# Performance work log

Measured on AMD Instinct MI355X. Metric: run time of the kernel, lower is better.

## Reference

```python
import jax, jax.numpy as jnp
import numpy as np

B, N = 8, 16384
NPOINT, RADIUS, NSAMPLE, IN_CH = 512, 0.5, 64, 6
EPS = 1e-5


def _sqdist(a, b):
    # a [B,S,3], b [B,N,3] -> [B,S,N] squared euclidean distances
    return (jnp.sum(a * a, -1)[:, :, None] + jnp.sum(b * b, -1)[:, None, :]
            - 2.0 * jnp.einsum('bsd,bnd->bsn', a, b))


def _fps(xyz, npoint):
    # farthest point sampling (deterministic: starts from index 0)
    Bb, Nn, _ = xyz.shape
    def body(carry, _):
        dist, far = carry  # dist [B,N], far [B]
        centroid = jnp.take_along_axis(xyz, far[:, None, None], axis=1)  # [B,1,3]
        d = jnp.sum((xyz - centroid) ** 2, -1)
        dist = jnp.minimum(dist, d)
        return (dist, jnp.argmax(dist, -1).astype(jnp.int32)), far
    init = (jnp.full((Bb, Nn), 1e10, xyz.dtype), jnp.zeros((Bb,), jnp.int32))
    _, idx = jax.lax.scan(body, init, None, length=npoint)
    return idx.T  # [B, npoint]


def _ball_query(radius, nsample, xyz, new_xyz):
    Nn = xyz.shape[1]
    sq = _sqdist(new_xyz, xyz)  # [B,S,N]
    gidx = jnp.where(sq > radius * radius, Nn,
                     jnp.arange(Nn, dtype=jnp.int32)[None, None, :])
    gidx = jnp.sort(gidx, axis=-1)[:, :, :nsample]  # [B,S,K]
    # pad slots (==N) get the first valid index, as in reference torch code
    return jnp.where(gidx == Nn, gidx[:, :, :1], gidx)


def _gather(x, idx):
    # x [B,N,C], idx [B,...] -> [B,...,C]
    return jax.vmap(lambda xb, ib: xb[ib])(x, idx)


def _forward(xyz, points, layers):
    fps_idx = _fps(xyz, NPOINT)
    new_xyz = _gather(xyz, fps_idx)                        # [B,S,3]
    idx = _ball_query(RADIUS, NSAMPLE, xyz, new_xyz)       # [B,S,K]
    grouped_xyz = _gather(xyz, idx) - new_xyz[:, :, None]  # [B,S,K,3]
    grouped_pts = _gather(points, idx)                     # [B,S,K,3]
    h = jnp.concatenate([grouped_xyz, grouped_pts], -1)[..., :IN_CH]  # [B,S,K,6]
    for (W, b, g, beta) in layers:
        # 1x1 Conv2d == per-point linear; BatchNorm2d (train mode) over (B,K,S)
        h = jnp.einsum('bskc,oc->bsko', h, W) + b
        mu = jnp.mean(h, axis=(0, 1, 2))
        var = jnp.var(h, axis=(0, 1, 2))
        h = jax.nn.relu(g * (h - mu) * jax.lax.rsqrt(var + EPS) + beta)
    return new_xyz, jnp.max(h, axis=2)  # [B,S,3], [B,S,C_out]


def setup_inputs() -> dict:
    key = jax.random.key(0)
    ks = jax.random.split(key, 4)
    return {
        'xyz': jax.random.normal(ks[0], (B, N, 3), jnp.float32),
        'points': jax.random.normal(ks[1], (B, N, 3), jnp.float32),
        'W0': jax.random.normal(ks[2], (64, IN_CH), jnp.float32) * (1.0 / np.sqrt(IN_CH)),
        'b0': jnp.zeros((64,), jnp.float32),
        'g0': jnp.ones((64,), jnp.float32),
        'beta0': jnp.zeros((64,), jnp.float32),
        'W1': jax.random.normal(ks[3], (128, 64), jnp.float32) * (1.0 / np.sqrt(64)),
        'b1': jnp.zeros((128,), jnp.float32),
        'g1': jnp.ones((128,), jnp.float32),
        'beta1': jnp.zeros((128,), jnp.float32),
    }


def reference(xyz, points, W0, b0, g0, beta0, W1, b1, g1, beta1):
    layers = [(W0, b0, g0, beta0), (W1, b1, g1, beta1)]
    return _forward(xyz, points, layers)
```

## Files before the change

### kernel.cpp

```cpp
#include <hip/hip_runtime.h>

#define NB    8
#define NPTS  16384
#define NS    512
#define NK    64
#define C1    64
#define C2    128
#define RAD2  0.25f
#define MTOT  (NB*NS*NK)

typedef float v2f __attribute__((ext_vector_type(2)));
typedef __bf16 bfv8 __attribute__((ext_vector_type(8)));
typedef float f32x4 __attribute__((ext_vector_type(4)));

extern __shared__ char dynsmem[];

#define UMAX_DPP(x, CTRL, RM)                                                   \
    do {                                                                        \
        unsigned _m = (unsigned)__builtin_amdgcn_update_dpp((int)(x), (int)(x), \
                                                            CTRL, RM, 0xf, false); \
        x = (x > _m) ? x : _m;                                                  \
    } while (0)
#define UMIN_DPP(x, CTRL, RM)                                                   \
    do {                                                                        \
        unsigned _m = (unsigned)__builtin_amdgcn_update_dpp((int)(x), (int)(x), \
                                                            CTRL, RM, 0xf, false); \
        x = (x < _m) ? x : _m;                                                  \
    } while (0)

__global__ __launch_bounds__(1024, 4) void fps_kernel(const float* __restrict__ xyz,
                                                      float* __restrict__ out) {
#pragma clang fp contract(off)
    int b = blockIdx.x;
    int tid = threadIdx.x;
    int lane = tid & 63;
    int w = tid >> 6;
    const float* base = xyz + (size_t)b * NPTS * 3;
    v2f* yv = (v2f*)dynsmem;
    v2f* zv = yv + 8192;
    __shared__ unsigned svals[2][16];
    __shared__ unsigned sidxs[2][16];
    v2f pxp[8], ddp[8];
#pragma unroll
    for (int jj = 0; jj < 8; ++jj) {
        int p0 = tid + (jj << 11);
        int p1 = p0 + 1024;
        float x0 = base[p0 * 3 + 0], y0 = base[p0 * 3 + 1], z0 = base[p0 * 3 + 2];
        float x1 = base[p1 * 3 + 0], y1 = base[p1 * 3 + 1], z1 = base[p1 * 3 + 2];
        pxp[jj].x = x0; pxp[jj].y = x1;
        v2f yp; yp.x = y0; yp.y = y1;
        v2f zp; zp.x = z0; zp.y = z1;
        yv[(jj << 10) + tid] = yp;
        zv[(jj << 10) + tid] = zp;
        ddp[jj].x = 1e10f; ddp[jj].y = 1e10f;
    }
    float cx = base[0], cy = base[1], cz = base[2];
    if (tid == 0) {
        float* o = out + (size_t)b * NS * 3;
        o[0] = cx; o[1] = cy; o[2] = cz;
    }
    __syncthreads();
    for (int i = 1; i < NS; ++i) {
        v2f cx2; cx2.x = cx; cx2.y = cx;
        v2f cy2; cy2.x = cy; cy2.y = cy;
        v2f cz2; cz2.x = cz; cz2.y = cz;
        v2f cm0, cm1, cm2, cm3;
        cm0.x = -1.f; cm0.y = -1.f; cm1 = cm0; cm2 = cm0; cm3 = cm0;
#pragma unroll
        for (int jj = 0; jj < 8; ++jj) {
            v2f yp = yv[(jj << 10) + tid];
            v2f zp = zv[(jj << 10) + tid];
            v2f dx = pxp[jj] - cx2;
            v2f dy = yp - cy2;
            v2f dz = zp - cz2;
            v2f d = (dx * dx + dy * dy) + dz * dz;
            v2f nd;
            nd.x = fminf(ddp[jj].x, d.x);
            nd.y = fminf(ddp[jj].y, d.y);
            ddp[jj] = nd;
            if ((jj & 3) == 0) { cm0.x = fmaxf(cm0.x, nd.x); cm0.y = fmaxf(cm0.y, nd.y); }
            if ((jj & 3) == 1) { cm1.x = fmaxf(cm1.x, nd.x); cm1.y = fmaxf(cm1.y, nd.y); }
            if ((jj & 3) == 2) { cm2.x = fmaxf(cm2.x, nd.x); cm2.y = fmaxf(cm2.y, nd.y); }
            if ((jj & 3) == 3) { cm3.x = fmaxf(cm3.x, nd.x); cm3.y = fmaxf(cm3.y, nd.y); }
        }
        v2f m01; m01.x = fmaxf(cm0.x, cm1.x); m01.y = fmaxf(cm0.y, cm1.y);
        v2f m23; m23.x = fmaxf(cm2.x, cm3.x); m23.y = fmaxf(cm2.y, cm3.y);
        float bv = fmaxf(fmaxf(m01.x, m23.x), fmaxf(m01.y, m23.y));
        unsigned vb = (unsigned)__float_as_int(bv);
        UMAX_DPP(vb, 0xB1, 0xf);
        UMAX_DPP(vb, 0x4E, 0xf);
        UMAX_DPP(vb, 0x141, 0xf);
        UMAX_DPP(vb, 0x140, 0xf);
        UMAX_DPP(vb, 0x142, 0xa);
        UMAX_DPP(vb, 0x143, 0xc);
        if (lane == 63) svals[i & 1][w] = vb;
        __syncthreads();
        unsigned wv = svals[i & 1][lane & 15];
        UMAX_DPP(wv, 0xB1, 0xf);
        UMAX_DPP(wv, 0x4E, 0xf);
        UMAX_DPP(wv, 0x141, 0xf);
        UMAX_DPP(wv, 0x140, 0xf);
        float W = __int_as_float((int)wv);
        unsigned lidx = 0x7fffffffu;
        if (__any(bv == W)) {
#pragma unroll
            for (int jj = 7; jj >= 0; --jj) {
                if (ddp[jj].y == W) lidx = (unsigned)(tid + (jj << 11) + 1024);
                if (ddp[jj].x == W) lidx = (unsigned)(tid + (jj << 11));
            }
        }
        UMIN_DPP(lidx, 0xB1, 0xf);
        UMIN_DPP(lidx, 0x4E, 0xf);
        UMIN_DPP(lidx, 0x141, 0xf);
        UMIN_DPP(lidx, 0x140, 0xf);
        UMIN_DPP(lidx, 0x142, 0xa);
        UMIN_DPP(lidx, 0x143, 0xc);
        if (lane == 63) sidxs[i & 1][w] = lidx;
        __syncthreads();
        unsigned ci = sidxs[i & 1][lane & 15];
        UMIN_DPP(ci, 0xB1, 0xf);
        UMIN_DPP(ci, 0x4E, 0xf);
        UMIN_DPP(ci, 0x141, 0xf);
        UMIN_DPP(ci, 0x140, 0xf);
        int ii = __builtin_amdgcn_readfirstlane((int)ci);
        const float* cp = base + (size_t)ii * 3;
        cx = cp[0]; cy = cp[1]; cz = cp[2];
        if (tid == 0) {
            float* o = out + ((size_t)b * NS + i) * 3;
            o[0] = cx; o[1] = cy; o[2] = cz;
        }
    }
}

__global__ __launch_bounds__(256) void ballq_kernel(const float* __restrict__ xyz,
                                                    const float* __restrict__ pts,
                                                    const float* __restrict__ newxyz,
                                                    float* __restrict__ feat) {
    int w = threadIdx.x >> 6;
    int lane = threadIdx.x & 63;
    int wid = blockIdx.x * 4 + w;
    int b = wid >> 9;
    const float* nx = newxyz + (size_t)wid * 3;
    float cx = nx[0], cy = nx[1], cz = nx[2];
    float sa = __fadd_rn(__fadd_rn(__fmul_rn(cx, cx), __fmul_rn(cy, cy)),
                         __fmul_rn(cz, cz));
    __shared__ int sidx[4][64];
    const float* base = xyz + (size_t)b * NPTS * 3;
    int cnt = 0;
    for (int off = 0; off < NPTS && cnt < NK; off += 64) {
        int p = off + lane;
        float bx = base[p * 3 + 0], by = base[p * 3 + 1], bz = base[p * 3 + 2];
        float sb = __fadd_rn(__fadd_rn(__fmul_rn(bx, bx), __fmul_rn(by, by)),
                             __fmul_rn(bz, bz));
        float dt = __fadd_rn(__fadd_rn(__fmul_rn(cx, bx), __fmul_rn(cy, by)),
                             __fmul_rn(cz, bz));
        float sq = __fsub_rn(__fadd_rn(sa, sb), __fmul_rn(2.0f, dt));
        bool inb = !(sq > RAD2);
        unsigned long long mask = __ballot(inb);
        int pos = cnt + (int)__popcll(mask & ((1ull << lane) - 1ull));
        if (inb && pos < NK) sidx[w][pos] = p;
        cnt += (int)__popcll(mask);
    }
    __syncthreads();
    int filled = cnt < NK ? cnt : NK;
    int sel = (lane < filled) ? lane : 0;
    int p = (filled > 0) ? sidx[w][sel] : 0;
    float gx = base[p * 3 + 0], gy = base[p * 3 + 1], gz = base[p * 3 + 2];
    const float* pb = pts + (size_t)b * NPTS * 3;
    float q0 = pb[p * 3 + 0], q1 = pb[p * 3 + 1], q2 = pb[p * 3 + 2];
    float* fr = feat + ((size_t)wid * NK + lane) * 6;
    fr[0] = __fsub_rn(gx, cx);
    fr[1] = __fsub_rn(gy, cy);
    fr[2] = __fsub_rn(gz, cz);
    fr[3] = q0; fr[4] = q1; fr[5] = q2;
}

__global__ __launch_bounds__(256) void stats0_kernel(const float* __restrict__ feat,
                                                     const float* __restrict__ W0,
                                                     const float* __restrict__ b0,
                                                     float* __restrict__ stats) {
    int lane = threadIdx.x & 63;
    int wid = blockIdx.x * 4 + (threadIdx.x >> 6);
    float w0[6];
#pragma unroll
    for (int j = 0; j < 6; ++j) w0[j] = W0[lane * 6 + j];
    float bb = b0[lane];
    float ssum = 0.f, ssq = 0.f;
    int r0 = wid * 256;
    for (int r = r0; r < r0 + 256; ++r) {
        const float* f = feat + (size_t)r * 6;
        float h = bb;
#pragma unroll
        for (int j = 0; j < 6; ++j) h = fmaf(w0[j], f[j], h);
        ssum += h;
        ssq = fmaf(h, h, ssq);
    }
    atomicAdd(&stats[lane], ssum);
    atomicAdd(&stats[64 + lane], ssq);
}

__device__ __forceinline__ void bf16_split(float v, unsigned short& hi, unsigned short& lo) {
    unsigned u = __float_as_uint(v);
    unsigned h = (u + 0x7fffu + ((u >> 16) & 1u)) >> 16;
    float rem = v - __uint_as_float(h << 16);
    unsigned ur = __float_as_uint(rem);
    unsigned l = (ur + 0x7fffu + ((ur >> 16) & 1u)) >> 16;
    hi = (unsigned short)h; lo = (unsigned short)l;
}

__global__ __launch_bounds__(256) void stats1_mfma_kernel(const float* __restrict__ feat,
                                                          const float* __restrict__ W0,
                                                          const float* __restrict__ b0,
                                                          const float* __restrict__ W1,
                                                          const float* __restrict__ b1,
                                                          const float* __restrict__ g0,
                                                          const float* __restrict__ be0,
                                                          float* __restrict__ stats) {
    char* lds = dynsmem;
    int tid = threadIdx.x;
    int lane = tid & 63;
    int w = tid >> 6;
    int g = blockIdx.x * 4 + w;
    for (int idx = tid; idx < 8192; idx += 256) {
        int o = idx >> 6, c = idx & 63;
        unsigned short hi, lo;
        bf16_split(W1[idx], hi, lo);
        int byt = (c * 2) ^ ((o & 7) << 4);
        *(unsigned short*)(lds + o * 128 + byt) = hi;
        *(unsigned short*)(lds + 16384 + o * 128 + byt) = lo;
    }
    const float inv = 1.0f / (float)MTOT;
    float mu0 = stats[lane] * inv;
    float var0 = fmaxf(stats[64 + lane] * inv - mu0 * mu0, 0.f);
    float a0 = g0[lane] * rsqrtf(var0 + 1e-5f);
    float c0v = fmaf(-mu0, a0, be0[lane]);
    float w0r[6];
#pragma unroll
    for (int j = 0; j < 6; ++j) w0r[j] = W0[lane * 6 + j];
    float b0v = b0[lane];
    char* X = lds + 32768 + w * 16384;
    __syncthreads();
    const float* fb = feat + (size_t)g * 64 * 6;
#pragma unroll 4
    for (int r = 0; r < 64; ++r) {
        const float* f = fb + r * 6;
        float h = b0v;
#pragma unroll
        for (int j = 0; j < 6; ++j) h = fmaf(w0r[j], f[j], h);
        float hn = fmaxf(fmaf(a0, h, c0v), 0.f);
        unsigned short hi, lo;
        bf16_split(hn, hi, lo);
        int byt = (lane * 2) ^ ((r & 7) << 4);
        *(unsigned short*)(X + r * 128 + byt) = hi;
        *(unsigned short*)(X + 8192 + r * 128 + byt) = lo;
    }
    __syncthreads();
    float b1v[8];
#pragma unroll
    for (int tn = 0; tn < 8; ++tn) b1v[tn] = b1[tn * 16 + (lane & 15)];
    float ssum[8], ssq[8];
#pragma unroll
    for (int tn = 0; tn < 8; ++tn) { ssum[tn] = 0.f; ssq[tn] = 0.f; }
#pragma unroll
    for (int tm = 0; tm < 4; ++tm) {
        bfv8 Ah[2], Al[2];
#pragma unroll
        for (int tk = 0; tk < 2; ++tk) {
            int r = tm * 16 + (lane & 15);
            int colb = (((lane >> 4) * 16) + tk * 64) ^ ((r & 7) << 4);
            Ah[tk] = *(const bfv8*)(X + r * 128 + colb);
            Al[tk] = *(const bfv8*)(X + 8192 + r * 128 + colb);
        }
#pragma unroll
        for (int tn = 0; tn < 8; ++tn) {
            int o = tn * 16 + (lane & 15);
            f32x4 acc = {0.f, 0.f, 0.f, 0.f};
#pragma unroll
            for (int tk = 0; tk < 2; ++tk) {
                int colb = (((lane >> 4) * 16) + tk * 64) ^ ((o & 7) << 4);
                bfv8 Bh = *(const bfv8*)(lds + o * 128 + colb);
                bfv8 Bl = *(const bfv8*)(lds + 16384 + o * 128 + colb);
                acc = __builtin_amdgcn_mfma_f32_16x16x32_bf16(Ah[tk], Bh, acc, 0, 0, 0);
                acc = __builtin_amdgcn_mfma_f32_16x16x32_bf16(Ah[tk], Bl, acc, 0, 0, 0);
                acc = __builtin_amdgcn_mfma_f32_16x16x32_bf16(Al[tk], Bh, acc, 0, 0, 0);
            }
#pragma unroll
            for (int j = 0; j < 4; ++j) {
                float h1 = acc[j] + b1v[tn];
                ssum[tn] += h1;
                ssq[tn] = fmaf(h1, h1, ssq[tn]);
            }
        }
    }
#pragma unroll
    for (int tn = 0; tn < 8; ++tn) {
        ssum[tn] += __shfl_xor(ssum[tn], 16);
        ssum[tn] += __shfl_xor(ssum[tn], 32);
        ssq[tn] += __shfl_xor(ssq[tn], 16);
        ssq[tn] += __shfl_xor(ssq[tn], 32);
    }
    __syncthreads();
    float* psum = (float*)(lds + 32768);
    float* psq  = (float*)(lds + 32768 + 4096);
    if (lane < 16) {
#pragma unroll
        for (int tn = 0; tn < 8; ++tn) {
            psum[w * 256 + tn * 16 + lane] = ssum[tn];
            psq[w * 256 + tn * 16 + lane] = ssq[tn];
        }
    }
    __syncthreads();
    {
        int ch = tid;
        if (ch < 128) {
            float s = psum[ch] + psum[256 + ch] + psum[512 + ch] + psum[768 + ch];
            float q = psq[ch] + psq[256 + ch] + psq[512 + ch] + psq[768 + ch];
            atomicAdd(&stats[128 + ch], s);
            atomicAdd(&stats[256 + ch], q);
        }
    }
}

__global__ __launch_bounds__(256) void final_mfma_kernel(const float* __restrict__ feat,
                                                         const float* __restrict__ W0,
                                                         const float* __restrict__ b0,
                                                         const float* __restrict__ W1,
                                                         const float* __restrict__ b1,
                                                         const float* __restrict__ g0,
                                                         const float* __restrict__ be0,
                                                         const float* __restrict__ g1,
                                                         const float* __restrict__ be1,
                                                         const float* __restrict__ stats,
                                                         float* __restrict__ out) {
    char* lds = dynsmem;
    int tid = threadIdx.x;
    int lane = tid & 63;
    int w = tid >> 6;
    int g = blockIdx.x * 4 + w;
    for (int idx = tid; idx < 8192; idx += 256) {
        int o = idx >> 6, c = idx & 63;
        unsigned short hi, lo;
        bf16_split(W1[idx], hi, lo);
        int byt = (c * 2) ^ ((o & 7) << 4);
        *(unsigned short*)(lds + o * 128 + byt) = hi;
        *(unsigned short*)(lds + 16384 + o * 128 + byt) = lo;
    }
    const float inv = 1.0f / (float)MTOT;
    float mu0 = stats[lane] * inv;
    float var0 = fmaxf(stats[64 + lane] * inv - mu0 * mu0, 0.f);
    float a0 = g0[lane] * rsqrtf(var0 + 1e-5f);
    float c0v = fmaf(-mu0, a0, be0[lane]);
    float w0r[6];
#pragma unroll
    for (int j = 0; j < 6; ++j) w0r[j] = W0[lane * 6 + j];
    float b0v = b0[lane];
    char* X = lds + 32768 + w * 16384;
    __syncthreads();
    const float* fb = feat + (size_t)g * 64 * 6;
#pragma unroll 4
    for (int r = 0; r < 64; ++r) {
        const float* f = fb + r * 6;
        float h = b0v;
#pragma unroll
        for (int j = 0; j < 6; ++j) h = fmaf(w0r[j], f[j], h);
        float hn = fmaxf(fmaf(a0, h, c0v), 0.f);
        unsigned short hi, lo;
        bf16_split(hn, hi, lo);
        int byt = (lane * 2) ^ ((r & 7) << 4);
        *(unsigned short*)(X + r * 128 + byt) = hi;
        *(unsigned short*)(X + 8192 + r * 128 + byt) = lo;
    }
    __syncthreads();
    float a1v[8], d1v[8];
#pragma unroll
    for (int tn = 0; tn < 8; ++tn) {
        int o = tn * 16 + (lane & 15);
        float mu1 = stats[128 + o] * inv;
        float var1 = fmaxf(stats[256 + o] * inv - mu1 * mu1, 0.f);
        float a1 = g1[o] * rsqrtf(var1 + 1e-5f);
        float c1 = fmaf(-mu1, a1, be1[o]);
        a1v[tn] = a1;
        d1v[tn] = fmaf(a1, b1[o], c1);
    }
    float mx[8];
#pragma unroll
    for (int tn = 0; tn < 8; ++tn) mx[tn] = -1e30f;
#pragma unroll
    for (int tm = 0; tm < 4; ++tm) {
        bfv8 Ah[2], Al[2];
#pragma unroll
        for (int tk = 0; tk < 2; ++tk) {
            int r = tm * 16 + (lane & 15);
            int colb = (((lane >> 4) * 16) + tk * 64) ^ ((r & 7) << 4);
            Ah[tk] = *(const bfv8*)(X + r * 128 + colb);
            Al[tk] = *(const bfv8*)(X + 8192 + r * 128 + colb);
        }
#pragma unroll
        for (int tn = 0; tn < 8; ++tn) {
            int o = tn * 16 + (lane & 15);
            f32x4 acc = {0.f, 0.f, 0.f, 0.f};
#pragma unroll
            for (int tk = 0; tk < 2; ++tk) {
                int colb = (((lane >> 4) * 16) + tk * 64) ^ ((o & 7) << 4);
                bfv8 Bh = *(const bfv8*)(lds + o * 128 + colb);
                bfv8 Bl = *(const bfv8*)(lds + 16384 + o * 128 + colb);
                acc = __builtin_amdgcn_mfma_f32_16x16x32_bf16(Ah[tk], Bh, acc, 0, 0, 0);
                acc = __builtin_amdgcn_mfma_f32_16x16x32_bf16(Ah[tk], Bl, acc, 0, 0, 0);
                acc = __builtin_amdgcn_mfma_f32_16x16x32_bf16(Al[tk], Bh, acc, 0, 0, 0);
            }
            float t0 = fmaxf(fmaf(a1v[tn], acc[0], d1v[tn]), 0.f);
            float t1 = fmaxf(fmaf(a1v[tn], acc[1], d1v[tn]), 0.f);
            float t2 = fmaxf(fmaf(a1v[tn], acc[2], d1v[tn]), 0.f);
            float t3 = fmaxf(fmaf(a1v[tn], acc[3], d1v[tn]), 0.f);
            mx[tn] = fmaxf(mx[tn], fmaxf(fmaxf(t0, t1), fmaxf(t2, t3)));
        }
    }
#pragma unroll
    for (int tn = 0; tn < 8; ++tn) {
        float v = mx[tn];
        v = fmaxf(v, __shfl_xor(v, 16));
        v = fmaxf(v, __shfl_xor(v, 32));
        mx[tn] = v;
    }
    if (lane < 16) {
        size_t ob = 12288 + (size_t)g * 128;
#pragma unroll
        for (int tn = 0; tn < 8; ++tn) out[ob + tn * 16 + lane] = mx[tn];
    }
}

extern "C" void kernel_launch(void* const* d_in, const int* in_sizes, int n_in,
                              void* d_out, int out_size, void* d_ws, size_t ws_size,
                              hipStream_t stream) {
    const float* xyz = (const float*)d_in[0];
    const float* pts = (const float*)d_in[1];
    const float* W0  = (const float*)d_in[2];
    const float* b0  = (const float*)d_in[3];
    const float* g0  = (const float*)d_in[4];
    const float* be0 = (const float*)d_in[5];
    const float* W1  = (const float*)d_in[6];
    const float* b1  = (const float*)d_in[7];
    const float* g1  = (const float*)d_in[8];
    const float* be1 = (const float*)d_in[9];
    float* out = (float*)d_out;

    float* feat  = (float*)d_ws;
    float* stats = feat + (size_t)MTOT * 6;

    const int fps_lds = 2 * NPTS * (int)sizeof(float);
    (void)hipFuncSetAttribute(reinterpret_cast<const void*>(fps_kernel),
                              hipFuncAttributeMaxDynamicSharedMemorySize, fps_lds);
    const int fm_lds = 98304;
    (void)hipFuncSetAttribute(reinterpret_cast<const void*>(stats1_mfma_kernel),
                              hipFuncAttributeMaxDynamicSharedMemorySize, fm_lds);
    (void)hipFuncSetAttribute(reinterpret_cast<const void*>(final_mfma_kernel),
                              hipFuncAttributeMaxDynamicSharedMemorySize, fm_lds);

    (void)hipMemsetAsync(stats, 0, 384 * sizeof(float), stream);
    fps_kernel<<<NB, 1024, fps_lds, stream>>>(xyz, out);
    ballq_kernel<<<1024, 256, 0, stream>>>(xyz, pts, out, feat);
    stats0_kernel<<<256, 256, 0, stream>>>(feat, W0, b0, stats);
    stats1_mfma_kernel<<<1024, 256, fm_lds, stream>>>(feat, W0, b0, W1, b1, g0, be0, stats);
    final_mfma_kernel<<<1024, 256, fm_lds, stream>>>(feat, W0, b0, W1, b1, g0, be0, g1, be1, stats, out);
}
```

Baseline: 1.064 ms.

## Derive layer-0 BatchNorm stats from input moments fused into ball query

Removes the separate stats0 kernel, which reread the whole feature buffer to compute per-channel sum and sum of squares of the first linear layer. The ball-query kernel now accumulates first and second moments of the 6-channel input (27 values) with DPP wave reductions and one atomic per block. The downstream kernels reconstruct layer-0 mean and variance algebraically from W0, b0 and these moments. This saves a kernel launch and a full pass over feat, at the cost of extra reductions in ball query and different floating-point accumulation, which may shift the variance slightly.

```diff
diff --git a/kernel.cpp b/kernel.cpp
--- a/kernel.cpp
+++ b/kernel.cpp
@@ -26,6 +26,12 @@
         unsigned _m = (unsigned)__builtin_amdgcn_update_dpp((int)(x), (int)(x), \
                                                             CTRL, RM, 0xf, false); \
         x = (x < _m) ? x : _m;                                                  \
+    } while (0)
+#define FSUM_DPP(x, CTRL, RM)                                                   \
+    do {                                                                        \
+        int _b = __builtin_amdgcn_update_dpp(0, __float_as_int(x), CTRL, RM,    \
+                                             0xf, false);                       \
+        x += __int_as_float(_b);                                                \
     } while (0)
 
 __global__ __launch_bounds__(1024, 4) void fps_kernel(const float* __restrict__ xyz,
@@ -135,7 +141,8 @@
 __global__ __launch_bounds__(256) void ballq_kernel(const float* __restrict__ xyz,
                                                     const float* __restrict__ pts,
                                                     const float* __restrict__ newxyz,
-                                                    float* __restrict__ feat) {
+                                                    float* __restrict__ feat,
+                                                    float* __restrict__ stats) {
     int w = threadIdx.x >> 6;
     int lane = threadIdx.x & 63;
     int wid = blockIdx.x * 4 + w;
@@ -145,6 +152,7 @@
     float sa = __fadd_rn(__fadd_rn(__fmul_rn(cx, cx), __fmul_rn(cy, cy)),
                          __fmul_rn(cz, cz));
     __shared__ int sidx[4][64];
+    __shared__ float pm[4][27];
     const float* base = xyz + (size_t)b * NPTS * 3;
     int cnt = 0;
     for (int off = 0; off < NPTS && cnt < NK; off += 64) {
@@ -167,36 +175,42 @@
     int p = (filled > 0) ? sidx[w][sel] : 0;
     float gx = base[p * 3 + 0], gy = base[p * 3 + 1], gz = base[p * 3 + 2];
     const float* pb = pts + (size_t)b * NPTS * 3;
-    float q0 = pb[p * 3 + 0], q1 = pb[p * 3 + 1], q2 = pb[p * 3 + 2];
+    float rowf[6];
+    rowf[0] = __fsub_rn(gx, cx);
+    rowf[1] = __fsub_rn(gy, cy);
+    rowf[2] = __fsub_rn(gz, cz);
+    rowf[3] = pb[p * 3 + 0];
+    rowf[4] = pb[p * 3 + 1];
+    rowf[5] = pb[p * 3 + 2];
     float* fr = feat + ((size_t)wid * NK + lane) * 6;
-    fr[0] = __fsub_rn(gx, cx);
-    fr[1] = __fsub_rn(gy, cy);
-    fr[2] = __fsub_rn(gz, cz);
-    fr[3] = q0; fr[4] = q1; fr[5] = q2;
-}
-
-__global__ __launch_bounds__(256) void stats0_kernel(const float* __restrict__ feat,
-                                                     const float* __restrict__ W0,
-                                                     const float* __restrict__ b0,
-                                                     float* __restrict__ stats) {
-    int lane = threadIdx.x & 63;
-    int wid = blockIdx.x * 4 + (threadIdx.x >> 6);
-    float w0[6];
-#pragma unroll
-    for (int j = 0; j < 6; ++j) w0[j] = W0[lane * 6 + j];
-    float bb = b0[lane];
-    float ssum = 0.f, ssq = 0.f;
-    int r0 = wid * 256;
-    for (int r = r0; r < r0 + 256; ++r) {
-        const float* f = feat + (size_t)r * 6;
-        float h = bb;
-#pragma unroll
-        for (int j = 0; j < 6; ++j) h = fmaf(w0[j], f[j], h);
-        ssum += h;
-        ssq = fmaf(h, h, ssq);
-    }
-    atomicAdd(&stats[lane], ssum);
-    atomicAdd(&stats[64 + lane], ssq);
+#pragma unroll
+    for (int j = 0; j < 6; ++j) fr[j] = rowf[j];
+    float mom[27];
+#pragma unroll
+    for (int j = 0; j < 6; ++j) mom[j] = rowf[j];
+    {
+        int t = 6;
+#pragma unroll
+        for (int j = 0; j < 6; ++j)
+#pragma unroll
+            for (int k = j; k < 6; ++k) mom[t++] = rowf[j] * rowf[k];
+    }
+#pragma unroll
+    for (int t = 0; t < 27; ++t) {
+        FSUM_DPP(mom[t], 0xB1, 0xf);
+        FSUM_DPP(mom[t], 0x4E, 0xf);
+        FSUM_DPP(mom[t], 0x141, 0xf);
+        FSUM_DPP(mom[t], 0x140, 0xf);
+        FSUM_DPP(mom[t], 0x142, 0xa);
+        FSUM_DPP(mom[t], 0x143, 0xc);
+        if (lane == 63) pm[w][t] = mom[t];
+    }
+    __syncthreads();
+    if (threadIdx.x < 27) {
+        int t = threadIdx.x;
+        float s = pm[0][t] + pm[1][t] + pm[2][t] + pm[3][t];
+        atomicAdd(&stats[t], s);
+    }
 }
 
 __device__ __forceinline__ void bf16_split(float v, unsigned short& hi, unsigned short& lo) {
@@ -206,6 +220,38 @@
     unsigned ur = __float_as_uint(rem);
     unsigned l = (ur + 0x7fffu + ((ur >> 16) & 1u)) >> 16;
     hi = (unsigned short)h; lo = (unsigned short)l;
+}
+
+__device__ __forceinline__ void bn0_from_moments(const float* __restrict__ stats,
+                                                 const float* __restrict__ g0,
+                                                 const float* __restrict__ be0,
+                                                 const float* w0r, float b0v,
+                                                 int lane, float& a0, float& c0v) {
+    const float inv = 1.0f / (float)MTOT;
+    float m6[6];
+#pragma unroll
+    for (int j = 0; j < 6; ++j) m6[j] = stats[j];
+    float s = 0.f;
+#pragma unroll
+    for (int j = 0; j < 6; ++j) s = fmaf(w0r[j], m6[j], s);
+    float quad = 0.f;
+    {
+        int t = 6;
+#pragma unroll
+        for (int j = 0; j < 6; ++j)
+#pragma unroll
+            for (int k = j; k < 6; ++k) {
+                float coef = w0r[j] * w0r[k];
+                if (j != k) coef = coef + coef;
+                quad = fmaf(coef, stats[t], quad);
+                ++t;
+            }
+    }
+    float mu0 = fmaf(s, inv, b0v);
+    float e2 = fmaf(quad, inv, fmaf(2.f * b0v * s, inv, b0v * b0v));
+    float var0 = fmaxf(e2 - mu0 * mu0, 0.f);
+    a0 = g0[lane] * rsqrtf(var0 + 1e-5f);
+    c0v = fmaf(-mu0, a0, be0[lane]);
 }
 
 __global__ __launch_bounds__(256) void stats1_mfma_kernel(const float* __restrict__ feat,
@@ -229,15 +275,12 @@
         *(unsigned short*)(lds + o * 128 + byt) = hi;
         *(unsigned short*)(lds + 16384 + o * 128 + byt) = lo;
     }
-    const float inv = 1.0f / (float)MTOT;
-    float mu0 = stats[lane] * inv;
-    float var0 = fmaxf(stats[64 + lane] * inv - mu0 * mu0, 0.f);
-    float a0 = g0[lane] * rsqrtf(var0 + 1e-5f);
-    float c0v = fmaf(-mu0, a0, be0[lane]);
     float w0r[6];
 #pragma unroll
     for (int j = 0; j < 6; ++j) w0r[j] = W0[lane * 6 + j];
     float b0v = b0[lane];
+    float a0, c0v;
+    bn0_from_moments(stats, g0, be0, w0r, b0v, lane, a0, c0v);
     char* X = lds + 32768 + w * 16384;
     __syncthreads();
     const float* fb = feat + (size_t)g * 64 * 6;
@@ -310,14 +353,12 @@
         }
     }
     __syncthreads();
-    {
+    if (tid < 128) {
         int ch = tid;
-        if (ch < 128) {
-            float s = psum[ch] + psum[256 + ch] + psum[512 + ch] + psum[768 + ch];
-            float q = psq[ch] + psq[256 + ch] + psq[512 + ch] + psq[768 + ch];
-            atomicAdd(&stats[128 + ch], s);
-            atomicAdd(&stats[256 + ch], q);
-        }
+        float s = psum[ch] + psum[256 + ch] + psum[512 + ch] + psum[768 + ch];
+        float q = psq[ch] + psq[256 + ch] + psq[512 + ch] + psq[768 + ch];
+        atomicAdd(&stats[128 + ch], s);
+        atomicAdd(&stats[256 + ch], q);
     }
 }
 
@@ -345,15 +386,12 @@
         *(unsigned short*)(lds + o * 128 + byt) = hi;
         *(unsigned short*)(lds + 16384 + o * 128 + byt) = lo;
     }
-    const float inv = 1.0f / (float)MTOT;
-    float mu0 = stats[lane] * inv;
-    float var0 = fmaxf(stats[64 + lane] * inv - mu0 * mu0, 0.f);
-    float a0 = g0[lane] * rsqrtf(var0 + 1e-5f);
-    float c0v = fmaf(-mu0, a0, be0[lane]);
     float w0r[6];
 #pragma unroll
     for (int j = 0; j < 6; ++j) w0r[j] = W0[lane * 6 + j];
     float b0v = b0[lane];
+    float a0, c0v;
+    bn0_from_moments(stats, g0, be0, w0r, b0v, lane, a0, c0v);
     char* X = lds + 32768 + w * 16384;
     __syncthreads();
     const float* fb = feat + (size_t)g * 64 * 6;
@@ -371,6 +409,7 @@
         *(unsigned short*)(X + 8192 + r * 128 + byt) = lo;
     }
     __syncthreads();
+    const float inv = 1.0f / (float)MTOT;
     float a1v[8], d1v[8];
 #pragma unroll
     for (int tn = 0; tn < 8; ++tn) {
@@ -458,8 +497,7 @@
 
     (void)hipMemsetAsync(stats, 0, 384 * sizeof(float), stream);
     fps_kernel<<<NB, 1024, fps_lds, stream>>>(xyz, out);
-    ballq_kernel<<<1024, 256, 0, stream>>>(xyz, pts, out, feat);
-    stats0_kernel<<<256, 256, 0, stream>>>(feat, W0, b0, stats);
+    ballq_kernel<<<1024, 256, 0, stream>>>(xyz, pts, out, feat, stats);
     stats1_mfma_kernel<<<1024, 256, fm_lds, stream>>>(feat, W0, b0, W1, b1, g0, be0, stats);
     final_mfma_kernel<<<1024, 256, fm_lds, stream>>>(feat, W0, b0, W1, b1, g0, be0, g1, be1, stats, out);
 }
```

Result: faster. 991.5 us (-6.8%).
